# Optimization experiments

Hardware: AMD Instinct MI355X
Metric: run time of the kernel (lower is better)

The kernel has to match this reference:

```python
import jax, jax.numpy as jnp
import numpy as np

EPS = 1e-5

def _bn(x, g, b, axes):
    # training-mode BatchNorm: biased batch stats over `axes`
    mu = jnp.mean(x, axis=axes, keepdims=True)
    var = jnp.var(x, axis=axes, keepdims=True)
    return (x - mu) * jax.lax.rsqrt(var + EPS) * g + b

def setup_inputs() -> dict:
    key = jax.random.key(0)
    ks = jax.random.split(key, 8)
    N, C, T, V = 32, 64, 512, 25
    H, D, BC = 3, 8, 16
    return {
        'x': jax.random.normal(ks[0], (N, C, T, V), jnp.float32),
        'A_topo': jax.random.uniform(ks[1], (H, V, V), jnp.float32),
        'ln_g': jnp.ones((C,), jnp.float32),
        'ln_b': jnp.zeros((C,), jnp.float32),
        'qk_w': jax.random.normal(ks[2], (2 * H * D, C), jnp.float32),
        'qk_b': jnp.zeros((2 * H * D,), jnp.float32),
        'convd_w': jax.random.normal(ks[3], (H, C, C), jnp.float32) * 0.05,
        'convd_b': jnp.zeros((H, C), jnp.float32),
        'sagc_bn_g': jnp.ones((C,), jnp.float32),
        'sagc_bn_b': jnp.zeros((C,), jnp.float32),
        'tcn_w1': jax.random.normal(ks[4], (4, BC, C), jnp.float32) * 0.1,
        'tcn_b1': jnp.zeros((4, BC), jnp.float32),
        'tcn_bn1_g': jnp.ones((4, BC), jnp.float32),
        'tcn_bn1_b': jnp.zeros((4, BC), jnp.float32),
        'tcn_w2': jax.random.normal(ks[5], (2, BC, BC, 5), jnp.float32) * 0.1,
        'tcn_b2': jnp.zeros((2, BC), jnp.float32),
        'tcn_bn2_g': jnp.ones((3, BC), jnp.float32),
        'tcn_bn2_b': jnp.zeros((3, BC), jnp.float32),
    }

def reference(x, A_topo, ln_g, ln_b, qk_w, qk_b, convd_w, convd_b,
              sagc_bn_g, sagc_bn_b, tcn_w1, tcn_b1, tcn_bn1_g, tcn_bn1_b,
              tcn_w2, tcn_b2, tcn_bn2_g, tcn_bn2_b):
    N, C, T, V = x.shape
    H = A_topo.shape[0]
    D = qk_w.shape[0] // (2 * H)
    scale = D ** -0.5

    # ---- SelfAttention ----
    feat = jnp.transpose(x, (0, 2, 3, 1))              # n t v c
    mu = feat.mean(-1, keepdims=True)
    var = feat.var(-1, keepdims=True)
    y = (feat - mu) * jax.lax.rsqrt(var + EPS) * ln_g + ln_b
    qk = y @ qk_w.T + qk_b                             # n t v 2HD
    q, k = jnp.split(qk, 2, axis=-1)
    q = q.reshape(N, T, V, H, D)
    k = k.reshape(N, T, V, H, D)
    dots = jnp.einsum('ntihd,ntjhd->nthij', q, k) * scale
    attn = jax.nn.softmax(dots, axis=-1)               # n t h v v

    # ---- SA_GC ----
    A = attn * A_topo                                  # broadcast (H,V,V)
    z = jnp.einsum('nthij,ntjc->nthic', A, feat)       # per-head A_h @ feature
    sa = jnp.einsum('nthic,hoc->noti', z, convd_w)     # fused per-head 1x1 convs
    sa = sa + convd_b.sum(0)[None, :, None, None]
    sa = _bn(sa, sagc_bn_g[None, :, None, None], sagc_bn_b[None, :, None, None], (0, 2, 3))
    y_gc = jax.nn.relu(sa + x)                         # down = identity (in==out)

    # ---- MultiScale_TemporalConv ----
    pre = jnp.einsum('nctv,koc->nkotv', y_gc, tcn_w1) + tcn_b1[None, :, :, None, None]
    pre = _bn(pre, tcn_bn1_g[None, :, :, None, None], tcn_bn1_b[None, :, :, None, None], (0, 3, 4))
    act = jax.nn.relu(pre[:, :3])                      # branches 0..2 get ReLU
    branches = []
    for i, d in enumerate((1, 2)):                     # dilated temporal convs
        pad = 2 * d                                    # (kernel-1)*d//2
        w = tcn_w2[i][:, :, :, None]                   # (O,I,5,1)
        zb = jax.lax.conv_general_dilated(
            act[:, i], w, (1, 1), ((pad, pad), (0, 0)), rhs_dilation=(d, 1),
            dimension_numbers=('NCHW', 'OIHW', 'NCHW'))
        zb = zb + tcn_b2[i][None, :, None, None]
        zb = _bn(zb, tcn_bn2_g[i][None, :, None, None], tcn_bn2_b[i][None, :, None, None], (0, 2, 3))
        branches.append(zb)
    p = jax.lax.reduce_window(act[:, 2], -jnp.inf, jax.lax.max,
                              (1, 1, 3, 1), (1, 1, 1, 1),
                              ((0, 0), (0, 0), (1, 1), (0, 0)))
    p = _bn(p, tcn_bn2_g[2][None, :, None, None], tcn_bn2_b[2][None, :, None, None], (0, 2, 3))
    branches.append(p)
    branches.append(pre[:, 3])                         # plain 1x1 branch
    tcn_out = jnp.concatenate(branches, axis=1)        # (N, C, T, V)

    # ---- EncodingBlock residual (identity: in==out, stride==1) ----
    return jax.nn.relu(tcn_out + x)
```

## Files before the change

### kernel.cpp

```cpp
#include <hip/hip_runtime.h>


#define EPS 1e-5f

typedef __bf16 bf16;
typedef __bf16 bf16x8 __attribute__((ext_vector_type(8)));
typedef float f32x4 __attribute__((ext_vector_type(4)));

__global__ void kprepack(const float* __restrict__ qk_w, const float* __restrict__ convd_w,
                         const float* __restrict__ w1g,
                         bf16* __restrict__ qkB, bf16* __restrict__ convB, bf16* __restrict__ w1B)
{
  int gid = blockIdx.x * 256 + threadIdx.x;
  if (gid < 384) {
    int lane = gid & 63, f = gid >> 6;
    int nt = f >> 1, ks = f & 1;
    int row = nt * 16 + (lane & 15);
    int col = ks * 32 + ((lane >> 4) * 8);
    const float* src = &qk_w[row * 64 + col];
    bf16* dh = &qkB[(f * 64 + lane) * 8];
    bf16* dl = dh + 3072;
    #pragma unroll
    for (int j = 0; j < 8; j++) {
      float w = src[j];
      bf16 h = (bf16)w;
      dh[j] = h;
      dl[j] = (bf16)(w - (float)h);
    }
  } else if (gid < 1920) {
    int g = gid - 384;
    int lane = g & 63, f = g >> 6;
    int nt = f / 6, ks = f - nt * 6;
    int k0 = ks * 32 + ((lane >> 4) * 8);
    int h = k0 >> 6, c = k0 & 63;
    int o = nt * 16 + (lane & 15);
    const float* src = &convd_w[(h * 64 + o) * 64 + c];
    bf16* d = &convB[(f * 64 + lane) * 8];
    #pragma unroll
    for (int j = 0; j < 8; j++) d[j] = (bf16)src[j];
  } else if (gid < 2432) {
    int g = gid - 1920;
    int lane = g & 63, f = g >> 6;
    int nt = f >> 1, ks = f & 1;
    int ko = nt * 16 + (lane & 15);
    int c0 = ks * 32 + ((lane >> 4) * 8);
    const float* src = &w1g[ko * 64 + c0];
    bf16* dh = &w1B[(f * 64 + lane) * 8];
    bf16* dl = dh + 4096;
    #pragma unroll
    for (int j = 0; j < 8; j++) {
      float w = src[j];
      bf16 h = (bf16)w;
      dh[j] = h;
      dl[j] = (bf16)(w - (float)h);
    }
  }
}

__global__ __launch_bounds__(256, 6)
void k1_sa_sagc(const float* __restrict__ x,
                const float* __restrict__ topo,
                const float* __restrict__ ln_g, const float* __restrict__ ln_b,
                const float* __restrict__ qk_b,
                const bf16* __restrict__ qkB, const bf16* __restrict__ convB,
                const float* __restrict__ convd_b,
                bf16* __restrict__ saB, float* __restrict__ pSum, float* __restrict__ pSq)
{
  const int t = blockIdx.x, n = blockIdx.y, tid = threadIdx.x;
  const int blk = n * 512 + t;
  const int lane = tid & 63, wave = tid >> 6;
  const int rr = lane & 15, co = (lane >> 4) * 8, rq = (lane >> 4) * 4;

  __shared__ __align__(16) float smem[6464];
  bf16*  featT = (bf16*)smem;
  bf16*  sAttn = (bf16*)(smem + 1280);
  float* sFeat = smem + 3200;
  float* sQK   = smem + 4900;
  bf16*  zL    = (bf16*)(smem + 3200);
  float* sMu   = smem + 6400;
  float* sRstd = smem + 6432;
  float* sSa   = smem;

  for (int idx = tid; idx < 1600; idx += 256) {
    int c = idx / 25, v = idx - c * 25;
    float f = x[((n * 64 + c) * 512 + t) * 25 + v];
    sFeat[v * 68 + c] = f;
    featT[c * 40 + v] = (bf16)f;
  }
  if (tid < 64) {
    #pragma unroll
    for (int j = 25; j < 32; j++) featT[tid * 40 + j] = (bf16)0.f;
  }
  __syncthreads();

  {
    int r = tid >> 3, sub = tid & 7;
    if (r < 25) {
      float s = 0.f, q = 0.f;
      #pragma unroll
      for (int c = 0; c < 64; c += 8) { float f = sFeat[r * 68 + c + sub]; s += f; q += f * f; }
      s += __shfl_xor(s, 1); q += __shfl_xor(q, 1);
      s += __shfl_xor(s, 2); q += __shfl_xor(q, 2);
      s += __shfl_xor(s, 4); q += __shfl_xor(q, 4);
      if (sub == 0) {
        float mu = s * (1.f / 64.f);
        float var = q * (1.f / 64.f) - mu * mu;
        sMu[r] = mu; sRstd[r] = rsqrtf(var + EPS);
      }
    }
  }
  __syncthreads();

  {
    const int mt = wave & 1;
    bf16x8 Ah[2], Al[2];
    int r0 = mt * 16 + rr;
    bool ok = r0 < 25;
    float mu = ok ? sMu[r0] : 0.f;
    float rs = ok ? sRstd[r0] : 0.f;
    #pragma unroll
    for (int ks = 0; ks < 2; ks++) {
      int c0 = ks * 32 + co;
      float4 fa = make_float4(0.f, 0.f, 0.f, 0.f), fb = fa;
      if (ok) { fa = *(const float4*)&sFeat[r0 * 68 + c0];
                fb = *(const float4*)&sFeat[r0 * 68 + c0 + 4]; }
      float4 g0  = *(const float4*)&ln_g[c0], g1  = *(const float4*)&ln_g[c0 + 4];
      float4 bb0 = *(const float4*)&ln_b[c0], bb1 = *(const float4*)&ln_b[c0 + 4];
      float y[8];
      y[0] = ok ? (fa.x - mu) * rs * g0.x + bb0.x : 0.f;
      y[1] = ok ? (fa.y - mu) * rs * g0.y + bb0.y : 0.f;
      y[2] = ok ? (fa.z - mu) * rs * g0.z + bb0.z : 0.f;
      y[3] = ok ? (fa.w - mu) * rs * g0.w + bb0.w : 0.f;
      y[4] = ok ? (fb.x - mu) * rs * g1.x + bb1.x : 0.f;
      y[5] = ok ? (fb.y - mu) * rs * g1.y + bb1.y : 0.f;
      y[6] = ok ? (fb.z - mu) * rs * g1.z + bb1.z : 0.f;
      y[7] = ok ? (fb.w - mu) * rs * g1.w + bb1.w : 0.f;
      #pragma unroll
      for (int j = 0; j < 8; j++) {
        bf16 h = (bf16)y[j];
        Ah[ks][j] = h;
        Al[ks][j] = (bf16)(y[j] - (float)h);
      }
    }
    #pragma unroll
    for (int q = 0; q < 2; q++) {
      if (wave >= 2 && q > 0) break;
      int nt = (wave < 2) ? (q * 2) : 1;
      float qb = qk_b[nt * 16 + rr];
      f32x4 acc = {qb, qb, qb, qb};
      #pragma unroll
      for (int ks = 0; ks < 2; ks++) {
        bf16x8 Bh = *(const bf16x8*)&qkB[((nt * 2 + ks) * 64 + lane) * 8];
        bf16x8 Bl = *(const bf16x8*)&qkB[3072 + ((nt * 2 + ks) * 64 + lane) * 8];
        acc = __builtin_amdgcn_mfma_f32_16x16x32_bf16(Ah[ks], Bh, acc, 0, 0, 0);
        acc = __builtin_amdgcn_mfma_f32_16x16x32_bf16(Ah[ks], Bl, acc, 0, 0, 0);
        acc = __builtin_amdgcn_mfma_f32_16x16x32_bf16(Al[ks], Bh, acc, 0, 0, 0);
      }
      #pragma unroll
      for (int r = 0; r < 4; r++) {
        int i = mt * 16 + rq + r;
        if (i < 25) sQK[i * 52 + nt * 16 + rr] = acc[r];
      }
    }
  }
  __syncthreads();

  if (tid < 150) {
    int p = tid >> 1, half = tid & 1;
    int h = p / 25, i = p - (p / 25) * 25;
    const float* qr = &sQK[i * 52 + h * 8];
    float4 qa = *(const float4*)qr, qb4 = *(const float4*)(qr + 4);
    const int j0 = half * 13;
    const int cnt = 13 - half;
    float lgv[13];
    float lmax = -3.4e38f;
    #pragma unroll
    for (int jj = 0; jj < 13; jj++) {
      int j = j0 + jj; j = j > 24 ? 24 : j;
      const float* kr = &sQK[j * 52 + 24 + h * 8];
      float4 ka = *(const float4*)kr, kb = *(const float4*)(kr + 4);
      float d = qa.x * ka.x + qa.y * ka.y + qa.z * ka.z + qa.w * ka.w
              + qb4.x * kb.x + qb4.y * kb.y + qb4.z * kb.z + qb4.w * kb.w;
      d *= 0.35355339059327373f;
      lgv[jj] = d;
      lmax = fmaxf(lmax, d);
    }
    lmax = fmaxf(lmax, __shfl_xor(lmax, 1));
    float se = 0.f;
    #pragma unroll
    for (int jj = 0; jj < 13; jj++) {
      float e = __expf(lgv[jj] - lmax);
      lgv[jj] = e;
      if (jj < cnt) se += e;
    }
    se += __shfl_xor(se, 1);
    float inv = 1.f / se;
    bf16* ar = &sAttn[(h * 32 + i) * 40];
    #pragma unroll
    for (int jj = 0; jj < 13; jj++) {
      int j = j0 + jj;
      if (jj < cnt) ar[j] = (bf16)(lgv[jj] * inv * topo[(h * 25 + i) * 25 + j]);
    }
    if (half) {
      #pragma unroll
      for (int j = 25; j < 32; j++) ar[j] = (bf16)0.f;
    }
  } else if (tid >= 192 && tid < 213) {
    int k = tid - 192;
    int h = k / 7, i = 25 + (k - (k / 7) * 7);
    bf16* ar = &sAttn[(h * 32 + i) * 40];
    #pragma unroll
    for (int j = 0; j < 32; j++) ar[j] = (bf16)0.f;
  }
  __syncthreads();

  {
    const int nt = wave;
    bf16x8 Bf = *(const bf16x8*)&featT[(nt * 16 + rr) * 40 + co];
    #pragma unroll
    for (int h = 0; h < 3; h++) {
      #pragma unroll
      for (int mt = 0; mt < 2; mt++) {
        bf16x8 Af = *(const bf16x8*)&sAttn[(h * 32 + mt * 16 + rr) * 40 + co];
        f32x4 az = {0.f, 0.f, 0.f, 0.f};
        az = __builtin_amdgcn_mfma_f32_16x16x32_bf16(Af, Bf, az, 0, 0, 0);
        #pragma unroll
        for (int r = 0; r < 4; r++)
          zL[(mt * 16 + rq + r) * 200 + h * 64 + nt * 16 + rr] = (bf16)az[r];
      }
    }
  }
  __syncthreads();

  {
    const int nt = wave;
    int o = nt * 16 + rr;
    float cb = convd_b[o] + convd_b[64 + o] + convd_b[128 + o];
    #pragma unroll
    for (int mt = 0; mt < 2; mt++) {
      f32x4 acc = {cb, cb, cb, cb};
      #pragma unroll
      for (int ks = 0; ks < 6; ks++) {
        bf16x8 Az = *(const bf16x8*)&zL[(mt * 16 + rr) * 200 + ks * 32 + co];
        bf16x8 Bw = *(const bf16x8*)&convB[((nt * 6 + ks) * 64 + lane) * 8];
        acc = __builtin_amdgcn_mfma_f32_16x16x32_bf16(Az, Bw, acc, 0, 0, 0);
      }
      #pragma unroll
      for (int r = 0; r < 4; r++) {
        int i = mt * 16 + rq + r;
        if (i < 25) sSa[o * 29 + i] = acc[r];
      }
    }
  }
  __syncthreads();

  if (tid < 200) {
    int lin = tid * 8;
    bf16x8 s8;
    #pragma unroll
    for (int e = 0; e < 8; e++) {
      int q = lin + e, o = q / 25, i2 = q - o * 25;
      s8[e] = (bf16)sSa[o * 29 + i2];
    }
    *(bf16x8*)&saB[blk * 1600 + lin] = s8;
  }
  if (tid < 64) {
    float s = 0.f, q = 0.f;
    #pragma unroll
    for (int i = 0; i < 25; i++) { float v = sSa[tid * 29 + i]; s += v; q += v * v; }
    pSum[blk * 64 + tid] = s;
    pSq [blk * 64 + tid] = q;
  }
}

__global__ __launch_bounds__(256, 4)
void kreduce(const float* __restrict__ pS, const float* __restrict__ pQ,
             int npart, int C, float invN,
             const float* __restrict__ g, const float* __restrict__ bta,
             float* __restrict__ sc, float* __restrict__ sh)
{
  int c = blockIdx.x, tid = threadIdx.x;
  float s = 0.f, q = 0.f;
  for (int i = tid; i < npart; i += 256) { s += pS[i * C + c]; q += pQ[i * C + c]; }
  #pragma unroll
  for (int m = 1; m < 64; m <<= 1) { s += __shfl_xor(s, m); q += __shfl_xor(q, m); }
  __shared__ float rs[4], rq[4];
  int w = tid >> 6;
  if ((tid & 63) == 0) { rs[w] = s; rq[w] = q; }
  __syncthreads();
  if (tid == 0) {
    float S = rs[0] + rs[1] + rs[2] + rs[3];
    float Q = rq[0] + rq[1] + rq[2] + rq[3];
    float mu = S * invN, var = Q * invN - mu * mu;
    float r = rsqrtf(var + EPS);
    sc[c] = g[c] * r;
    sh[c] = bta[c] - mu * g[c] * r;
  }
}

__global__ __launch_bounds__(256, 8)
void k3_ygc_pre(const float* __restrict__ x, const bf16* __restrict__ saB,
                const float* __restrict__ scS, const float* __restrict__ shS,
                const bf16* __restrict__ w1B, const float* __restrict__ b1,
                bf16* __restrict__ preB, float* __restrict__ pSum, float* __restrict__ pSq)
{
  const int t = blockIdx.x, n = blockIdx.y, tid = threadIdx.x;
  const int blk = n * 512 + t;
  const int lane = tid & 63, wave = tid >> 6;
  const int rr = lane & 15, co = (lane >> 4) * 8, rq = (lane >> 4) * 4;

  __shared__ __align__(16) float sYgc[25 * 68];
  __shared__ float sPre[64 * 29];

  if (tid < 200) {
    int lin = tid * 8;
    bf16x8 s8 = *(const bf16x8*)&saB[blk * 1600 + lin];
    #pragma unroll
    for (int e = 0; e < 8; e++) {
      int q = lin + e, c = q / 25, v = q - c * 25;
      float val = scS[c] * (float)s8[e] + shS[c] + x[((n * 64 + c) * 512 + t) * 25 + v];
      sYgc[v * 68 + c] = fmaxf(val, 0.f);
    }
  }
  __syncthreads();

  {
    const int nt = wave;
    bf16x8 Ah[2][2], Al[2][2];
    #pragma unroll
    for (int mt = 0; mt < 2; mt++) {
      int r0 = mt * 16 + rr;
      bool ok = r0 < 25;
      #pragma unroll
      for (int ks = 0; ks < 2; ks++) {
        float v[8];
        if (ok) {
          float4 fa = *(const float4*)&sYgc[r0 * 68 + ks * 32 + co];
          float4 fb = *(const float4*)&sYgc[r0 * 68 + ks * 32 + co + 4];
          v[0]=fa.x; v[1]=fa.y; v[2]=fa.z; v[3]=fa.w;
          v[4]=fb.x; v[5]=fb.y; v[6]=fb.z; v[7]=fb.w;
        } else {
          #pragma unroll
          for (int j = 0; j < 8; j++) v[j] = 0.f;
        }
        #pragma unroll
        for (int j = 0; j < 8; j++) {
          bf16 h = (bf16)v[j];
          Ah[mt][ks][j] = h;
          Al[mt][ks][j] = (bf16)(v[j] - (float)h);
        }
      }
    }
    float bb = b1[nt * 16 + rr];
    #pragma unroll
    for (int mt = 0; mt < 2; mt++) {
      f32x4 acc = {bb, bb, bb, bb};
      #pragma unroll
      for (int ks = 0; ks < 2; ks++) {
        bf16x8 Bh = *(const bf16x8*)&w1B[((nt * 2 + ks) * 64 + lane) * 8];
        bf16x8 Bl = *(const bf16x8*)&w1B[4096 + ((nt * 2 + ks) * 64 + lane) * 8];
        acc = __builtin_amdgcn_mfma_f32_16x16x32_bf16(Ah[mt][ks], Bh, acc, 0, 0, 0);
        acc = __builtin_amdgcn_mfma_f32_16x16x32_bf16(Ah[mt][ks], Bl, acc, 0, 0, 0);
        acc = __builtin_amdgcn_mfma_f32_16x16x32_bf16(Al[mt][ks], Bh, acc, 0, 0, 0);
      }
      #pragma unroll
      for (int r = 0; r < 4; r++) {
        int i = mt * 16 + rq + r;
        if (i < 25) sPre[(nt * 16 + rr) * 29 + i] = acc[r];
      }
    }
  }
  __syncthreads();

  if (tid < 200) {
    int lin = tid * 8;
    bf16x8 p8;
    #pragma unroll
    for (int e = 0; e < 8; e++) {
      int q = lin + e, ko = q / 25, v = q - ko * 25;
      p8[e] = (bf16)sPre[ko * 29 + v];
    }
    *(bf16x8*)&preB[blk * 1600 + lin] = p8;
  }
  if (tid < 64) {
    float s = 0.f, q = 0.f;
    #pragma unroll
    for (int i = 0; i < 25; i++) { float v = sPre[tid * 29 + i]; s += v; q += v * v; }
    pSum[blk * 64 + tid] = s;
    pSq [blk * 64 + tid] = q;
  }
}

template<int D>
__device__ __forceinline__ void conv5(const float* __restrict__ sIn, const float* __restrict__ sW,
                                      float4 bias, int o4, int v, int tb, float acc[8][4])
{
  #pragma unroll
  for (int s = 0; s < 8; s++) {
    acc[s][0] = bias.x; acc[s][1] = bias.y; acc[s][2] = bias.z; acc[s][3] = bias.w;
  }
  const int NW = 8 + 4 * D;
  for (int ic = 0; ic < 16; ic++) {
    float4 wk[5];
    #pragma unroll
    for (int kt = 0; kt < 5; kt++) wk[kt] = *(const float4*)&sW[(ic * 5 + kt) * 16 + o4];
    float xw[8 + 4 * D];
    #pragma unroll
    for (int w = 0; w < NW; w++) xw[w] = sIn[(ic * 24 + (tb - 2 * D + w + 4)) * 25 + v];
    #pragma unroll
    for (int s = 0; s < 8; s++)
      #pragma unroll
      for (int kt = 0; kt < 5; kt++) {
        float xv = xw[s + kt * D];
        acc[s][0] += xv * wk[kt].x; acc[s][1] += xv * wk[kt].y;
        acc[s][2] += xv * wk[kt].z; acc[s][3] += xv * wk[kt].w;
      }
  }
}

__global__ __launch_bounds__(256, 2)
void k5_tcn_branch(const bf16* __restrict__ preB,
                   const float* __restrict__ sc1, const float* __restrict__ sh1,
                   const float* __restrict__ w2, const float* __restrict__ b2,
                   bf16* __restrict__ zbB, float* __restrict__ pSum2, float* __restrict__ pSq2)
{
  const int tt = blockIdx.x, b = blockIdx.y, n = blockIdx.z;
  const int tid = threadIdx.x, t0 = tt * 16;
  __shared__ __align__(16) float sIn[16 * 24 * 25];
  __shared__ __align__(16) float sW[16 * 5 * 16];
  __shared__ float sRedS[4][4][4], sRedQ[4][4][4];

  for (int idx = tid; idx < 1200; idx += 256) {
    int r = idx / 50, k8 = idx - r * 50;
    int gt = t0 - 4 + r;
    int lin = k8 * 8;
    if (gt >= 0 && gt < 512) {
      bf16x8 p8 = *(const bf16x8*)&preB[((n * 512 + gt) * 64 + b * 16) * 25 + lin];
      #pragma unroll
      for (int e = 0; e < 8; e++) {
        int q = lin + e, ic = q / 25, v = q - ic * 25;
        int ch = b * 16 + ic;
        sIn[(ic * 24 + r) * 25 + v] = fmaxf(sc1[ch] * (float)p8[e] + sh1[ch], 0.f);
      }
    } else {
      #pragma unroll
      for (int e = 0; e < 8; e++) {
        int q = lin + e, ic = q / 25, v = q - ic * 25;
        sIn[(ic * 24 + r) * 25 + v] = 0.f;
      }
    }
  }
  if (b < 2)
    for (int idx = tid; idx < 1280; idx += 256) {
      int o = idx / 80, rem = idx - o * 80;
      int ic = rem / 5, kt = rem - ic * 5;
      sW[(ic * 5 + kt) * 16 + o] = w2[((b * 16 + o) * 16 + ic) * 5 + kt];
    }
  __syncthreads();

  float po[4] = {0.f, 0.f, 0.f, 0.f}, pq[4] = {0.f, 0.f, 0.f, 0.f};
  if (tid < 200) {
    int tx = tid & 3, o4 = tx * 4;
    int g = tid >> 2;
    int v = g % 25, th = g / 25;
    int tb = th * 8;
    float acc[8][4];
    if (b == 0)      conv5<1>(sIn, sW, *(const float4*)&b2[o4],      o4, v, tb, acc);
    else if (b == 1) conv5<2>(sIn, sW, *(const float4*)&b2[16 + o4], o4, v, tb, acc);
    else {
      #pragma unroll
      for (int s = 0; s < 8; s++)
        #pragma unroll
        for (int j = 0; j < 4; j++) {
          int o = o4 + j, r = tb + s + 4;
          float a = sIn[(o * 24 + r - 1) * 25 + v];
          float m = sIn[(o * 24 + r    ) * 25 + v];
          float c = sIn[(o * 24 + r + 1) * 25 + v];
          acc[s][j] = fmaxf(fmaxf(a, m), c);
        }
    }
    #pragma unroll
    for (int s = 0; s < 8; s++) {
      int gt = t0 + tb + s;
      #pragma unroll
      for (int j = 0; j < 4; j++) {
        float val = acc[s][j];
        zbB[(((b * 32 + n) * 512 + gt) * 16 + (o4 + j)) * 25 + v] = (bf16)val;
        po[j] += val; pq[j] += val * val;
      }
    }
  }
  #pragma unroll
  for (int m = 4; m < 64; m <<= 1) {
    #pragma unroll
    for (int j = 0; j < 4; j++) { po[j] += __shfl_xor(po[j], m); pq[j] += __shfl_xor(pq[j], m); }
  }
  int lane = tid & 63, w = tid >> 6;
  if (lane < 4) {
    #pragma unroll
    for (int j = 0; j < 4; j++) { sRedS[w][lane][j] = po[j]; sRedQ[w][lane][j] = pq[j]; }
  }
  __syncthreads();
  if (tid < 16) {
    int o = tid, txo = o >> 2, j = o & 3;
    float s = 0.f, q = 0.f;
    #pragma unroll
    for (int ww = 0; ww < 4; ww++) { s += sRedS[ww][txo][j]; q += sRedQ[ww][txo][j]; }
    int pidx = (n * 32 + tt) * 48 + b * 16 + o;
    pSum2[pidx] = s; pSq2[pidx] = q;
  }
}

__global__ __launch_bounds__(256, 8)
void k7_final(const float* __restrict__ x, const bf16* __restrict__ preB,
              const bf16* __restrict__ zbB,
              const float* __restrict__ sc1, const float* __restrict__ sh1,
              const float* __restrict__ sc2, const float* __restrict__ sh2,
              float* __restrict__ out)
{
  const int bid = blockIdx.x;
  const int n = bid >> 6, tc = bid & 63;
  const int t0 = tc * 8;
  for (int e = threadIdx.x; e < 12800; e += 256) {
    int ch = e / 200, r = e - ch * 200;
    int tl = r / 25, v = r - tl * 25;
    int t = t0 + tl;
    int b = ch >> 4, o = ch & 15;
    float val;
    if (b < 3) {
      val = sc2[b * 16 + o] * (float)zbB[(((b * 32 + n) * 512 + t) * 16 + o) * 25 + v]
          + sh2[b * 16 + o];
    } else {
      int ko = 48 + o;
      val = sc1[ko] * (float)preB[((n * 512 + t) * 64 + ko) * 25 + v] + sh1[ko];
    }
    int ax = (n * 64 + ch) * 12800 + t * 25 + v;
    out[ax] = fmaxf(val + x[ax], 0.f);
  }
}

extern "C" void kernel_launch(void* const* d_in, const int* in_sizes, int n_in,
                              void* d_out, int out_size, void* d_ws, size_t ws_size,
                              hipStream_t stream)
{
  const float* x       = (const float*)d_in[0];
  const float* topo    = (const float*)d_in[1];
  const float* ln_g    = (const float*)d_in[2];
  const float* ln_b    = (const float*)d_in[3];
  const float* qk_w    = (const float*)d_in[4];
  const float* qk_b    = (const float*)d_in[5];
  const float* convd_w = (const float*)d_in[6];
  const float* convd_b = (const float*)d_in[7];
  const float* sagc_g  = (const float*)d_in[8];
  const float* sagc_b  = (const float*)d_in[9];
  const float* w1      = (const float*)d_in[10];
  const float* b1      = (const float*)d_in[11];
  const float* bn1_g   = (const float*)d_in[12];
  const float* bn1_b   = (const float*)d_in[13];
  const float* w2      = (const float*)d_in[14];
  const float* b2      = (const float*)d_in[15];
  const float* bn2_g   = (const float*)d_in[16];
  const float* bn2_b   = (const float*)d_in[17];
  float* out = (float*)d_out;
  float* ws  = (float*)d_ws;

  bf16*  preB  = (bf16*)ws;
  bf16*  zbB   = (bf16*)(ws + 13107200);
  float* pSum1 = ws + 22937600;
  float* pSq1  = ws + 23986176;
  float* pSum2 = ws + 25034752;
  float* pSq2  = ws + 25083904;
  float* scS   = ws + 25133056;  float* shS = scS + 64;
  float* sc1   = scS + 128;      float* sh1 = scS + 192;
  float* sc2   = scS + 256;      float* sh2 = scS + 304;
  bf16*  qkB   = (bf16*)(ws + 25133440);
  bf16*  convB = (bf16*)(ws + 25136512);
  bf16*  w1B   = (bf16*)(ws + 25142656);
  bf16*  saB   = (bf16*)d_out;

  const float invN = 1.f / 409600.f;

  kprepack<<<10, 256, 0, stream>>>(qk_w, convd_w, w1, qkB, convB, w1B);
  k1_sa_sagc<<<dim3(512, 32), 256, 0, stream>>>(x, topo, ln_g, ln_b, qk_b,
                                                qkB, convB, convd_b, saB, pSum1, pSq1);
  kreduce<<<64, 256, 0, stream>>>(pSum1, pSq1, 16384, 64, invN, sagc_g, sagc_b, scS, shS);
  k3_ygc_pre<<<dim3(512, 32), 256, 0, stream>>>(x, saB, scS, shS, w1B, b1,
                                                preB, pSum1, pSq1);
  kreduce<<<64, 256, 0, stream>>>(pSum1, pSq1, 16384, 64, invN, bn1_g, bn1_b, sc1, sh1);
  k5_tcn_branch<<<dim3(32, 3, 32), 256, 0, stream>>>(preB, sc1, sh1, w2, b2,
                                                     zbB, pSum2, pSq2);
  kreduce<<<48, 256, 0, stream>>>(pSum2, pSq2, 1024, 48, invN, bn2_g, bn2_b, sc2, sh2);
  k7_final<<<2048, 256, 0, stream>>>(x, preB, zbB, sc1, sh1, sc2, sh2, out);
}
```

Measured before the change: 406.1 us.

## Restructure LN staging, presplit bf16 operands in LDS, add two-stage stat reduction

k1 now loads x with coalesced per-channel-group threads, computes LayerNorm stats from partial sums in LDS, and writes the normalized hi/lo bf16 split directly into LDS. The MFMA A-operands are then plain vector loads instead of per-wave recomputation. k3 does the same hi/lo presplit for its input. The 16384-row BN partial reduction becomes a parallel two-stage pass: a new kpart kernel followed by a smaller kreduce. Launch bounds are also changed (k1 from 6 to 5, k5 from 2 to 3), which trades occupancy against register headroom and adds one extra kernel launch per reduction.

```diff
diff --git a/kernel.cpp b/kernel.cpp
--- a/kernel.cpp
+++ b/kernel.cpp
@@ -57,7 +57,7 @@
   }
 }
 
-__global__ __launch_bounds__(256, 6)
+__global__ __launch_bounds__(256, 5)
 void k1_sa_sagc(const float* __restrict__ x,
                 const float* __restrict__ topo,
                 const float* __restrict__ ln_g, const float* __restrict__ ln_b,
@@ -71,76 +71,61 @@
   const int lane = tid & 63, wave = tid >> 6;
   const int rr = lane & 15, co = (lane >> 4) * 8, rq = (lane >> 4) * 4;
 
-  __shared__ __align__(16) float smem[6464];
-  bf16*  featT = (bf16*)smem;
-  bf16*  sAttn = (bf16*)(smem + 1280);
-  float* sFeat = smem + 3200;
-  float* sQK   = smem + 4900;
-  bf16*  zL    = (bf16*)(smem + 3200);
-  float* sMu   = smem + 6400;
-  float* sRstd = smem + 6432;
-  float* sSa   = smem;
-
-  for (int idx = tid; idx < 1600; idx += 256) {
-    int c = idx / 25, v = idx - c * 25;
-    float f = x[((n * 64 + c) * 512 + t) * 25 + v];
-    sFeat[v * 68 + c] = f;
-    featT[c * 40 + v] = (bf16)f;
-  }
-  if (tid < 64) {
-    #pragma unroll
-    for (int j = 25; j < 32; j++) featT[tid * 40 + j] = (bf16)0.f;
-  }
-  __syncthreads();
-
+  __shared__ __align__(16) float smem[7928];
+  bf16*  featT  = (bf16*)smem;
+  bf16*  yH     = (bf16*)(smem + 1280);
+  bf16*  yL     = (bf16*)(smem + 2180);
+  bf16*  zL     = (bf16*)(smem + 1280);
+  float* sPartS = smem + 4480;
+  float* sPartQ = smem + 4580;
+  float* sQK    = smem + 4480;
+  bf16*  sAttn  = (bf16*)(smem + 5880);
+  float* sSa    = smem + 4480;
+  float* sLnG   = smem + 7800;
+  float* sLnB   = smem + 7864;
+
+  const int v = tid & 31, cb = tid >> 5;
+  float xv[8];
   {
-    int r = tid >> 3, sub = tid & 7;
-    if (r < 25) {
-      float s = 0.f, q = 0.f;
-      #pragma unroll
-      for (int c = 0; c < 64; c += 8) { float f = sFeat[r * 68 + c + sub]; s += f; q += f * f; }
-      s += __shfl_xor(s, 1); q += __shfl_xor(q, 1);
-      s += __shfl_xor(s, 2); q += __shfl_xor(q, 2);
-      s += __shfl_xor(s, 4); q += __shfl_xor(q, 4);
-      if (sub == 0) {
-        float mu = s * (1.f / 64.f);
-        float var = q * (1.f / 64.f) - mu * mu;
-        sMu[r] = mu; sRstd[r] = rsqrtf(var + EPS);
-      }
+    const float* xp = &x[((n * 64 + cb) * 512 + t) * 25 + (v < 25 ? v : 0)];
+    float s = 0.f, q = 0.f;
+    #pragma unroll
+    for (int k = 0; k < 8; k++) {
+      float f = (v < 25) ? xp[k * 102400] : 0.f;
+      xv[k] = f;
+      featT[(cb + 8 * k) * 40 + v] = (bf16)f;
+      s += f; q += f * f;
+    }
+    s += __shfl_xor(s, 32); q += __shfl_xor(q, 32);
+    if (lane < 32 && v < 25) { sPartS[v * 4 + wave] = s; sPartQ[v * 4 + wave] = q; }
+    if (tid < 64) { sLnG[tid] = ln_g[tid]; sLnB[tid] = ln_b[tid]; }
+  }
+  __syncthreads();
+
+  if (v < 25) {
+    float S = sPartS[v * 4] + sPartS[v * 4 + 1] + sPartS[v * 4 + 2] + sPartS[v * 4 + 3];
+    float Q = sPartQ[v * 4] + sPartQ[v * 4 + 1] + sPartQ[v * 4 + 2] + sPartQ[v * 4 + 3];
+    float mu = S * (1.f / 64.f);
+    float rstd = rsqrtf(Q * (1.f / 64.f) - mu * mu + EPS);
+    #pragma unroll
+    for (int k = 0; k < 8; k++) {
+      int c = cb + 8 * k;
+      float yv = (xv[k] - mu) * rstd * sLnG[c] + sLnB[c];
+      bf16 h = (bf16)yv;
+      yH[v * 72 + c] = h;
+      yL[v * 72 + c] = (bf16)(yv - (float)h);
     }
   }
   __syncthreads();
 
   {
     const int mt = wave & 1;
+    const int r0 = mt * 16 + rr;
     bf16x8 Ah[2], Al[2];
-    int r0 = mt * 16 + rr;
-    bool ok = r0 < 25;
-    float mu = ok ? sMu[r0] : 0.f;
-    float rs = ok ? sRstd[r0] : 0.f;
     #pragma unroll
     for (int ks = 0; ks < 2; ks++) {
-      int c0 = ks * 32 + co;
-      float4 fa = make_float4(0.f, 0.f, 0.f, 0.f), fb = fa;
-      if (ok) { fa = *(const float4*)&sFeat[r0 * 68 + c0];
-                fb = *(const float4*)&sFeat[r0 * 68 + c0 + 4]; }
-      float4 g0  = *(const float4*)&ln_g[c0], g1  = *(const float4*)&ln_g[c0 + 4];
-      float4 bb0 = *(const float4*)&ln_b[c0], bb1 = *(const float4*)&ln_b[c0 + 4];
-      float y[8];
-      y[0] = ok ? (fa.x - mu) * rs * g0.x + bb0.x : 0.f;
-      y[1] = ok ? (fa.y - mu) * rs * g0.y + bb0.y : 0.f;
-      y[2] = ok ? (fa.z - mu) * rs * g0.z + bb0.z : 0.f;
-      y[3] = ok ? (fa.w - mu) * rs * g0.w + bb0.w : 0.f;
-      y[4] = ok ? (fb.x - mu) * rs * g1.x + bb1.x : 0.f;
-      y[5] = ok ? (fb.y - mu) * rs * g1.y + bb1.y : 0.f;
-      y[6] = ok ? (fb.z - mu) * rs * g1.z + bb1.z : 0.f;
-      y[7] = ok ? (fb.w - mu) * rs * g1.w + bb1.w : 0.f;
-      #pragma unroll
-      for (int j = 0; j < 8; j++) {
-        bf16 h = (bf16)y[j];
-        Ah[ks][j] = h;
-        Al[ks][j] = (bf16)(y[j] - (float)h);
-      }
+      Ah[ks] = *(const bf16x8*)&yH[r0 * 72 + ks * 32 + co];
+      Al[ks] = *(const bf16x8*)&yL[r0 * 72 + ks * 32 + co];
     }
     #pragma unroll
     for (int q = 0; q < 2; q++) {
@@ -159,7 +144,7 @@
       #pragma unroll
       for (int r = 0; r < 4; r++) {
         int i = mt * 16 + rq + r;
-        if (i < 25) sQK[i * 52 + nt * 16 + rr] = acc[r];
+        if (i < 25) sQK[i * 56 + nt * 16 + rr] = acc[r];
       }
     }
   }
@@ -168,7 +153,7 @@
   if (tid < 150) {
     int p = tid >> 1, half = tid & 1;
     int h = p / 25, i = p - (p / 25) * 25;
-    const float* qr = &sQK[i * 52 + h * 8];
+    const float* qr = &sQK[i * 56 + h * 8];
     float4 qa = *(const float4*)qr, qb4 = *(const float4*)(qr + 4);
     const int j0 = half * 13;
     const int cnt = 13 - half;
@@ -177,7 +162,7 @@
     #pragma unroll
     for (int jj = 0; jj < 13; jj++) {
       int j = j0 + jj; j = j > 24 ? 24 : j;
-      const float* kr = &sQK[j * 52 + 24 + h * 8];
+      const float* kr = &sQK[j * 56 + 24 + h * 8];
       float4 ka = *(const float4*)kr, kb = *(const float4*)(kr + 4);
       float d = qa.x * ka.x + qa.y * ka.y + qa.z * ka.z + qa.w * ka.w
               + qb4.x * kb.x + qb4.y * kb.y + qb4.z * kb.z + qb4.w * kb.w;
@@ -235,10 +220,10 @@
   {
     const int nt = wave;
     int o = nt * 16 + rr;
-    float cb = convd_b[o] + convd_b[64 + o] + convd_b[128 + o];
+    float cb2 = convd_b[o] + convd_b[64 + o] + convd_b[128 + o];
     #pragma unroll
     for (int mt = 0; mt < 2; mt++) {
-      f32x4 acc = {cb, cb, cb, cb};
+      f32x4 acc = {cb2, cb2, cb2, cb2};
       #pragma unroll
       for (int ks = 0; ks < 6; ks++) {
         bf16x8 Az = *(const bf16x8*)&zL[(mt * 16 + rr) * 200 + ks * 32 + co];
@@ -267,9 +252,29 @@
   if (tid < 64) {
     float s = 0.f, q = 0.f;
     #pragma unroll
-    for (int i = 0; i < 25; i++) { float v = sSa[tid * 29 + i]; s += v; q += v * v; }
+    for (int i = 0; i < 25; i++) { float v2 = sSa[tid * 29 + i]; s += v2; q += v2 * v2; }
     pSum[blk * 64 + tid] = s;
     pSq [blk * 64 + tid] = q;
+  }
+}
+
+__global__ __launch_bounds__(256, 8)
+void kpart(const float* __restrict__ pS, const float* __restrict__ pQ,
+           float* __restrict__ oS, float* __restrict__ oQ)
+{
+  const int g = blockIdx.x, tid = threadIdx.x;
+  const int c = tid & 63, r = tid >> 6;
+  float s = 0.f, q = 0.f;
+  for (int i = 0; i < 16; i++) {
+    int b = g * 64 + r * 16 + i;
+    s += pS[b * 64 + c]; q += pQ[b * 64 + c];
+  }
+  __shared__ float ls[4][64], lq[4][64];
+  ls[r][c] = s; lq[r][c] = q;
+  __syncthreads();
+  if (tid < 64) {
+    oS[g * 64 + tid] = ls[0][tid] + ls[1][tid] + ls[2][tid] + ls[3][tid];
+    oQ[g * 64 + tid] = lq[0][tid] + lq[1][tid] + lq[2][tid] + lq[3][tid];
   }
 }
 
@@ -309,17 +314,23 @@
   const int lane = tid & 63, wave = tid >> 6;
   const int rr = lane & 15, co = (lane >> 4) * 8, rq = (lane >> 4) * 4;
 
-  __shared__ __align__(16) float sYgc[25 * 68];
-  __shared__ float sPre[64 * 29];
+  __shared__ __align__(16) float smem[3656];
+  bf16*  yH   = (bf16*)smem;
+  bf16*  yL   = (bf16*)(smem + 900);
+  float* sPre = smem + 1800;
 
   if (tid < 200) {
     int lin = tid * 8;
+    int c = lin / 25, v = lin - c * 25;
     bf16x8 s8 = *(const bf16x8*)&saB[blk * 1600 + lin];
     #pragma unroll
     for (int e = 0; e < 8; e++) {
-      int q = lin + e, c = q / 25, v = q - c * 25;
       float val = scS[c] * (float)s8[e] + shS[c] + x[((n * 64 + c) * 512 + t) * 25 + v];
-      sYgc[v * 68 + c] = fmaxf(val, 0.f);
+      val = fmaxf(val, 0.f);
+      bf16 h = (bf16)val;
+      yH[v * 72 + c] = h;
+      yL[v * 72 + c] = (bf16)(val - (float)h);
+      if (++v == 25) { v = 0; c++; }
     }
   }
   __syncthreads();
@@ -330,25 +341,10 @@
     #pragma unroll
     for (int mt = 0; mt < 2; mt++) {
       int r0 = mt * 16 + rr;
-      bool ok = r0 < 25;
       #pragma unroll
       for (int ks = 0; ks < 2; ks++) {
-        float v[8];
-        if (ok) {
-          float4 fa = *(const float4*)&sYgc[r0 * 68 + ks * 32 + co];
-          float4 fb = *(const float4*)&sYgc[r0 * 68 + ks * 32 + co + 4];
-          v[0]=fa.x; v[1]=fa.y; v[2]=fa.z; v[3]=fa.w;
-          v[4]=fb.x; v[5]=fb.y; v[6]=fb.z; v[7]=fb.w;
-        } else {
-          #pragma unroll
-          for (int j = 0; j < 8; j++) v[j] = 0.f;
-        }
-        #pragma unroll
-        for (int j = 0; j < 8; j++) {
-          bf16 h = (bf16)v[j];
-          Ah[mt][ks][j] = h;
-          Al[mt][ks][j] = (bf16)(v[j] - (float)h);
-        }
+        Ah[mt][ks] = *(const bf16x8*)&yH[r0 * 72 + ks * 32 + co];
+        Al[mt][ks] = *(const bf16x8*)&yL[r0 * 72 + ks * 32 + co];
       }
     }
     float bb = b1[nt * 16 + rr];
@@ -418,7 +414,7 @@
   }
 }
 
-__global__ __launch_bounds__(256, 2)
+__global__ __launch_bounds__(256, 3)
 void k5_tcn_branch(const bf16* __restrict__ preB,
                    const float* __restrict__ sc1, const float* __restrict__ sh1,
                    const float* __restrict__ w2, const float* __restrict__ b2,
@@ -576,6 +572,8 @@
   bf16*  qkB   = (bf16*)(ws + 25133440);
   bf16*  convB = (bf16*)(ws + 25136512);
   bf16*  w1B   = (bf16*)(ws + 25142656);
+  float* oS1   = ws + 25146752;
+  float* oQ1   = ws + 25163136;
   bf16*  saB   = (bf16*)d_out;
 
   const float invN = 1.f / 409600.f;
@@ -583,10 +581,12 @@
   kprepack<<<10, 256, 0, stream>>>(qk_w, convd_w, w1, qkB, convB, w1B);
   k1_sa_sagc<<<dim3(512, 32), 256, 0, stream>>>(x, topo, ln_g, ln_b, qk_b,
                                                 qkB, convB, convd_b, saB, pSum1, pSq1);
-  kreduce<<<64, 256, 0, stream>>>(pSum1, pSq1, 16384, 64, invN, sagc_g, sagc_b, scS, shS);
+  kpart<<<256, 256, 0, stream>>>(pSum1, pSq1, oS1, oQ1);
+  kreduce<<<64, 256, 0, stream>>>(oS1, oQ1, 256, 64, invN, sagc_g, sagc_b, scS, shS);
   k3_ygc_pre<<<dim3(512, 32), 256, 0, stream>>>(x, saB, scS, shS, w1B, b1,
                                                 preB, pSum1, pSq1);
-  kreduce<<<64, 256, 0, stream>>>(pSum1, pSq1, 16384, 64, invN, bn1_g, bn1_b, sc1, sh1);
+  kpart<<<256, 256, 0, stream>>>(pSum1, pSq1, oS1, oQ1);
+  kreduce<<<64, 256, 0, stream>>>(oS1, oQ1, 256, 64, invN, bn1_g, bn1_b, sc1, sh1);
   k5_tcn_branch<<<dim3(32, 3, 32), 256, 0, stream>>>(preB, sc1, sh1, w2, b2,
                                                      zbB, pSum2, pSq2);
   kreduce<<<48, 256, 0, stream>>>(pSum2, pSq2, 1024, 48, invN, bn2_g, bn2_b, sc2, sh2);
```

Measured after the change: 364.2 us. 1.11x faster.
